# Kernel optimization log

Measured on AMD Instinct MI355X. Metric: run time of the kernel, lower is better.

The kernel has to match this reference:

```python
import jax, jax.numpy as jnp
import numpy as np

HIDDEN = 1024
HEADS = 16
HEAD_DIM = HIDDEN // HEADS
EPS = 1e-5


def setup_inputs() -> dict:
    key = jax.random.key(0)
    ks = jax.random.split(key, 9)
    B, S, H = 2, 2048, HIDDEN
    scale = 1.0 / np.sqrt(H)
    inp = {
        "hidden_states": jax.random.normal(ks[0], (B, S, H), dtype=jnp.float32),
        "Wq": jax.random.normal(ks[1], (H, H), dtype=jnp.float32) * scale,
        "bq": jnp.zeros((H,), jnp.float32),
        "Wk": jax.random.normal(ks[2], (H, H), dtype=jnp.float32) * scale,
        "bk": jnp.zeros((H,), jnp.float32),
        "Wv": jax.random.normal(ks[3], (H, H), dtype=jnp.float32) * scale,
        "bv": jnp.zeros((H,), jnp.float32),
        "Wo": jax.random.normal(ks[4], (H, H), dtype=jnp.float32) * scale,
        "bo": jnp.zeros((H,), jnp.float32),
        "gamma": jnp.ones((H,), jnp.float32),
        "beta": jnp.zeros((H,), jnp.float32),
    }
    return inp


def reference(hidden_states, Wq, bq, Wk, bk, Wv, bv, Wo, bo, gamma, beta):
    B, S, H = hidden_states.shape
    residual = hidden_states

    def shape(x):  # [B,S,H] -> [B,heads,S,head_dim]
        return x.reshape(B, S, HEADS, HEAD_DIM).transpose(0, 2, 1, 3)

    q = shape(hidden_states @ Wq + bq)
    k = shape(hidden_states @ Wk + bk)
    v = shape(hidden_states @ Wv + bv)

    scores = jnp.einsum("bhqd,bhkd->bhqk", q, k) / jnp.sqrt(
        jnp.asarray(HEAD_DIM, hidden_states.dtype))
    probs = jax.nn.softmax(scores, axis=-1)
    context = jnp.einsum("bhqk,bhkd->bhqd", probs, v)
    context = context.transpose(0, 2, 1, 3).reshape(B, S, H)

    output = context @ Wo + bo
    x = output + residual
    mu = jnp.mean(x, axis=-1, keepdims=True)
    var = jnp.mean(jnp.square(x - mu), axis=-1, keepdims=True)
    return (x - mu) * jax.lax.rsqrt(var + EPS) * gamma + beta
```

## Files before the change

kernel.cpp:

```cpp
#include <hip/hip_runtime.h>
#include <hip/hip_bf16.h>
#include <math.h>

#define HIDDEN 1024
#define HEADS 16
#define HEAD_DIM 64
#define EPS 1e-5f

typedef __attribute__((ext_vector_type(8))) short bf16x8;
typedef __attribute__((ext_vector_type(4))) float f32x4;

#if defined(__has_builtin)
#if __has_builtin(__builtin_amdgcn_exp2f)
#define EXP2(x) __builtin_amdgcn_exp2f(x)
#endif
#endif
#ifndef EXP2
#define EXP2(x) exp2f(x)
#endif

#define QSCALE 0.18033688011112042f

__device__ __forceinline__ short f2bf(float f) {
    union { float f; unsigned u; } v; v.f = f;
    unsigned r = v.u + 0x7fffu + ((v.u >> 16) & 1u);
    return (short)(r >> 16);
}

__device__ __forceinline__ void gl_lds16(const void* g, void* l) {
    __builtin_amdgcn_global_load_lds(
        (const __attribute__((address_space(1))) void*)g,
        (__attribute__((address_space(3))) void*)l, 16, 0, 0);
}

__global__ __launch_bounds__(256) void prep_kernel(
    const float* __restrict__ X,
    const float* __restrict__ Wq, const float* __restrict__ Wk,
    const float* __restrict__ Wv, const float* __restrict__ Wo,
    const float* __restrict__ bq, const float* __restrict__ bk,
    const float* __restrict__ bv,
    short* __restrict__ Xb, short* __restrict__ Wt3, short* __restrict__ Wot,
    float* __restrict__ b3)
{
    __shared__ short tile[32][33];
    const int id = blockIdx.x;
    if (id < 4096) {
        int i = id * 1024 + threadIdx.x * 4;
        float4 v = *(const float4*)(X + i);
        short o[4] = { f2bf(v.x), f2bf(v.y), f2bf(v.z), f2bf(v.w) };
        *(uint2*)(Xb + i) = *(uint2*)o;
    } else if (id < 8192) {
        int t = id - 4096;
        const int wsel = t >> 10; t &= 1023;
        const float* W = (wsel == 0) ? Wq : (wsel == 1) ? Wk : (wsel == 2) ? Wv : Wo;
        short* dst = (wsel < 3) ? (Wt3 + (size_t)wsel * 1024 * 1024) : Wot;
        const float scale = (wsel == 0) ? QSCALE : 1.0f;
        int n0 = (t & 31) * 32;
        int k0 = (t >> 5) * 32;
        int tx = threadIdx.x & 31;
        int ty = threadIdx.x >> 5;
        #pragma unroll
        for (int i = 0; i < 32; i += 8)
            tile[ty + i][tx] = f2bf(W[(size_t)(k0 + ty + i) * 1024 + n0 + tx] * scale);
        __syncthreads();
        #pragma unroll
        for (int i = 0; i < 32; i += 8)
            dst[(size_t)(n0 + ty + i) * 1024 + k0 + tx] = tile[tx][ty + i];
    } else {
        int i = (id - 8192) * 256 + threadIdx.x;
        if (i < 3072) {
            float v = (i < 1024) ? bq[i] * QSCALE
                    : (i < 2048) ? bk[i - 1024] : bv[i - 2048];
            b3[i] = v;
        }
    }
}

__global__ __launch_bounds__(256) void gemm_bt_mfma(
    const short* __restrict__ A, const short* __restrict__ Bt,
    const float* __restrict__ bias,
    void* __restrict__ C0, int ldc0,
    void* __restrict__ C1, int split_col, int ldc1, int v_transpose,
    const float* __restrict__ resid,
    int M, int N, int K, int out_bf16)
{
    __shared__ short As[128 * 32];
    __shared__ short Bs[128 * 32];
    const int tid = threadIdx.x;
    const int wave = tid >> 6, lane = tid & 63;
    const int ln16 = lane & 15, quad = lane >> 4;
    const int wm = (wave >> 1) * 64, wn = (wave & 1) * 64;
    const int brow = blockIdx.y * 128, bcol = blockIdx.x * 128;

    const int sr  = lane >> 2;
    const int scb = lane & 3;

    f32x4 acc[4][4];
    #pragma unroll
    for (int mt = 0; mt < 4; ++mt)
        #pragma unroll
        for (int nt = 0; nt < 4; ++nt) acc[mt][nt] = (f32x4){0.f, 0.f, 0.f, 0.f};

    for (int k0 = 0; k0 < K; k0 += 32) {
        __syncthreads();
        #pragma unroll
        for (int i = 0; i < 2; ++i) {
            int rb = i * 64 + wave * 16;
            int r  = rb + sr;
            int csrc = (scb ^ ((r >> 1) & 3)) * 8;
            gl_lds16(A  + (size_t)(brow + r) * K + k0 + csrc, &As[rb * 32]);
            gl_lds16(Bt + (size_t)(bcol + r) * K + k0 + csrc, &Bs[rb * 32]);
        }
        __syncthreads();

        bf16x8 af[4], bf[4];
        #pragma unroll
        for (int mt = 0; mt < 4; ++mt) {
            int r = wm + mt * 16 + ln16;
            af[mt] = *(const bf16x8*)&As[r * 32 + ((quad ^ ((r >> 1) & 3)) * 8)];
        }
        #pragma unroll
        for (int nt = 0; nt < 4; ++nt) {
            int r = wn + nt * 16 + ln16;
            bf[nt] = *(const bf16x8*)&Bs[r * 32 + ((quad ^ ((r >> 1) & 3)) * 8)];
        }
        #pragma unroll
        for (int mt = 0; mt < 4; ++mt)
            #pragma unroll
            for (int nt = 0; nt < 4; ++nt)
                acc[mt][nt] = __builtin_amdgcn_mfma_f32_16x16x32_bf16(
                    af[mt], bf[nt], acc[mt][nt], 0, 0, 0);
    }

    if (v_transpose && bcol >= split_col) {
        #pragma unroll
        for (int mt = 0; mt < 4; ++mt) {
            int row0 = brow + wm + mt * 16 + quad * 4;
            #pragma unroll
            for (int nt = 0; nt < 4; ++nt) {
                int col = bcol + wn + nt * 16 + ln16;
                int feat = col - split_col;
                float bz = bias[col];
                short pk[4];
                #pragma unroll
                for (int r = 0; r < 4; ++r) pk[r] = f2bf(acc[mt][nt][r] + bz);
                *(uint2*)((short*)C1 + (size_t)feat * ldc1 + row0) = *(uint2*)pk;
            }
        }
        return;
    }

    void* Cp = C0; int ld = ldc0; int coff = 0;
    if (bcol >= split_col) { Cp = C1; ld = ldc1; coff = split_col; }

    #pragma unroll
    for (int mt = 0; mt < 4; ++mt) {
        #pragma unroll
        for (int r = 0; r < 4; ++r) {
            int row = brow + wm + mt * 16 + quad * 4 + r;
            #pragma unroll
            for (int nt = 0; nt < 4; ++nt) {
                int col = bcol + wn + nt * 16 + ln16;
                float v = acc[mt][nt][r] + bias[col];
                if (resid) v += resid[(size_t)row * N + col];
                if (out_bf16) ((short*)Cp)[(size_t)row * ld + (col - coff)] = f2bf(v);
                else          ((float*)Cp)[(size_t)row * ld + (col - coff)] = v;
            }
        }
    }
}

__global__ __launch_bounds__(256) void attn_mfma_kernel(
    const short* __restrict__ QKb, const short* __restrict__ VT,
    short* __restrict__ Ctx)
{
    const int S = 2048;
    const int h = blockIdx.x, qt = blockIdx.y, b = blockIdx.z;
    const int tid = threadIdx.x;
    const int wave = tid >> 6, lane = tid & 63;
    const int ln16 = lane & 15, quad = lane >> 4;
    const int qh = wave >> 1, kh = wave & 1;

    __shared__ short Ks[2][64 * 64];
    __shared__ short Vs[2][64 * 64];
    __shared__ short Ps[256 * 72];
    __shared__ float Ls[128];

    const int qbase = b * S + qt * 128 + qh * 64;
    bf16x8 qfrag[4][2];
    #pragma unroll
    for (int qg = 0; qg < 4; ++qg)
        #pragma unroll
        for (int kb = 0; kb < 2; ++kb)
            qfrag[qg][kb] = *(const bf16x8*)(QKb +
                (size_t)(qbase + qg * 16 + ln16) * 2048 + h * 64 + kb * 32 + quad * 8);

    bf16x8 ones;
    #pragma unroll
    for (int j = 0; j < 8; ++j) ones[j] = (short)0x3F80;

    f32x4 of[4][4], lacc[4];
    #pragma unroll
    for (int qg = 0; qg < 4; ++qg) {
        lacc[qg] = (f32x4){0.f, 0.f, 0.f, 0.f};
        #pragma unroll
        for (int nt = 0; nt < 4; ++nt) of[qg][nt] = (f32x4){0.f, 0.f, 0.f, 0.f};
    }

    const int st  = wave >> 1;
    const int skv = wave & 1;
    const int sr  = lane >> 3;
    const int scb = lane & 7;

    for (int p = 0; p < 16; ++p) {
        __syncthreads();
        #pragma unroll
        for (int c = 0; c < 8; ++c) {
            int r = c * 8 + sr;
            int csrc = (scb ^ (r & 7)) * 8;
            int ktp = 2 * p + st;
            if (skv == 0) {
                gl_lds16(QKb + (size_t)(b * S + ktp * 64 + r) * 2048
                             + 1024 + h * 64 + csrc,
                         &Ks[st][c * 512]);
            } else {
                gl_lds16(VT + (size_t)(h * 64 + r) * 4096
                            + b * S + ktp * 64 + csrc,
                         &Vs[st][c * 512]);
            }
        }
        __syncthreads();

        #pragma unroll
        for (int nt = 0; nt < 4; ++nt) {
            bf16x8 kf[2];
            #pragma unroll
            for (int kb = 0; kb < 2; ++kb) {
                int r = nt * 16 + ln16;
                int cb = (kb * 4 + quad) ^ (r & 7);
                kf[kb] = *(const bf16x8*)&Ks[kh][r * 64 + cb * 8];
            }
            #pragma unroll
            for (int qg = 0; qg < 4; ++qg) {
                f32x4 a = (f32x4){0.f, 0.f, 0.f, 0.f};
                a = __builtin_amdgcn_mfma_f32_16x16x32_bf16(kf[0], qfrag[qg][0], a, 0, 0, 0);
                a = __builtin_amdgcn_mfma_f32_16x16x32_bf16(kf[1], qfrag[qg][1], a, 0, 0, 0);
                float p0 = EXP2(a[0]), p1 = EXP2(a[1]);
                float p2 = EXP2(a[2]), p3 = EXP2(a[3]);
                union { __hip_bfloat162 h2; unsigned u; } c01, c23;
                c01.h2 = __float22bfloat162_rn(make_float2(p0, p1));
                c23.h2 = __float22bfloat162_rn(make_float2(p2, p3));
                uint2 w; w.x = c01.u; w.y = c23.u;
                *(uint2*)&Ps[(wave * 64 + qg * 16 + ln16) * 72 + nt * 16 + quad * 4] = w;
            }
        }

        bf16x8 pf[4][2];
        #pragma unroll
        for (int qg = 0; qg < 4; ++qg)
            #pragma unroll
            for (int kb = 0; kb < 2; ++kb)
                pf[qg][kb] = *(const bf16x8*)
                    &Ps[(wave * 64 + qg * 16 + ln16) * 72 + kb * 32 + quad * 8];

        #pragma unroll
        for (int qg = 0; qg < 4; ++qg) {
            lacc[qg] = __builtin_amdgcn_mfma_f32_16x16x32_bf16(pf[qg][0], ones, lacc[qg], 0, 0, 0);
            lacc[qg] = __builtin_amdgcn_mfma_f32_16x16x32_bf16(pf[qg][1], ones, lacc[qg], 0, 0, 0);
        }
        #pragma unroll
        for (int nt = 0; nt < 4; ++nt) {
            bf16x8 vf[2];
            #pragma unroll
            for (int kb = 0; kb < 2; ++kb) {
                int r = nt * 16 + ln16;
                int cb = (kb * 4 + quad) ^ (r & 7);
                vf[kb] = *(const bf16x8*)&Vs[kh][r * 64 + cb * 8];
            }
            #pragma unroll
            for (int qg = 0; qg < 4; ++qg) {
                of[qg][nt] = __builtin_amdgcn_mfma_f32_16x16x32_bf16(pf[qg][0], vf[0], of[qg][nt], 0, 0, 0);
                of[qg][nt] = __builtin_amdgcn_mfma_f32_16x16x32_bf16(pf[qg][1], vf[1], of[qg][nt], 0, 0, 0);
            }
        }
    }

    float* Os = (float*)Ps;
    float* OsQ = Os + qh * (64 * 66);
    __syncthreads();
    if (kh == 1) {
        #pragma unroll
        for (int qg = 0; qg < 4; ++qg) {
            #pragma unroll
            for (int r = 0; r < 4; ++r) {
                int ql = qg * 16 + quad * 4 + r;
                #pragma unroll
                for (int nt = 0; nt < 4; ++nt)
                    OsQ[ql * 66 + nt * 16 + ln16] = of[qg][nt][r];
                if (ln16 == 0) Ls[qh * 64 + ql] = lacc[qg][r];
            }
        }
    }
    __syncthreads();
    if (kh == 0) {
        #pragma unroll
        for (int qg = 0; qg < 4; ++qg) {
            #pragma unroll
            for (int r = 0; r < 4; ++r) {
                int ql = qg * 16 + quad * 4 + r;
                float inv = 1.f / (lacc[qg][r] + Ls[qh * 64 + ql]);
                int row = qbase + ql;
                #pragma unroll
                for (int nt = 0; nt < 4; ++nt) {
                    float v = of[qg][nt][r] + OsQ[ql * 66 + nt * 16 + ln16];
                    Ctx[(size_t)row * 1024 + h * 64 + nt * 16 + ln16] = f2bf(v * inv);
                }
            }
        }
    }
}

__global__ __launch_bounds__(256) void resln_kernel(
    const float* __restrict__ xin, const float* __restrict__ gamma,
    const float* __restrict__ beta, float* __restrict__ out)
{
    const int row = blockIdx.x;
    const int tid = threadIdx.x;
    const int wid = tid >> 6, lane = tid & 63;
    __shared__ float red[8];

    float4 x = *(const float4*)(xin + (size_t)row * HIDDEN + tid * 4);
    float s = x.x + x.y + x.z + x.w;
    #pragma unroll
    for (int off = 32; off > 0; off >>= 1) s += __shfl_xor(s, off, 64);
    if (lane == 0) red[wid] = s;
    __syncthreads();
    float mu = (red[0] + red[1] + red[2] + red[3]) * (1.f / HIDDEN);

    float dx = x.x - mu, dy = x.y - mu, dz = x.z - mu, dw = x.w - mu;
    float v = dx * dx + dy * dy + dz * dz + dw * dw;
    #pragma unroll
    for (int off = 32; off > 0; off >>= 1) v += __shfl_xor(v, off, 64);
    if (lane == 0) red[4 + wid] = v;
    __syncthreads();
    float var = (red[4] + red[5] + red[6] + red[7]) * (1.f / HIDDEN);
    float rstd = rsqrtf(var + EPS);

    float4 g = *(const float4*)(gamma + tid * 4);
    float4 bt = *(const float4*)(beta + tid * 4);
    float4 o;
    o.x = dx * rstd * g.x + bt.x;
    o.y = dy * rstd * g.y + bt.y;
    o.z = dz * rstd * g.z + bt.z;
    o.w = dw * rstd * g.w + bt.w;
    *(float4*)(out + (size_t)row * HIDDEN + tid * 4) = o;
}

extern "C" void kernel_launch(void* const* d_in, const int* in_sizes, int n_in,
                              void* d_out, int out_size, void* d_ws, size_t ws_size,
                              hipStream_t stream)
{
    const float* X     = (const float*)d_in[0];
    const float* Wq    = (const float*)d_in[1];
    const float* bq    = (const float*)d_in[2];
    const float* Wk    = (const float*)d_in[3];
    const float* bk    = (const float*)d_in[4];
    const float* Wv    = (const float*)d_in[5];
    const float* bv    = (const float*)d_in[6];
    const float* Wo    = (const float*)d_in[7];
    const float* bo    = (const float*)d_in[8];
    const float* gamma = (const float*)d_in[9];
    const float* beta  = (const float*)d_in[10];
    float* out = (float*)d_out;

    const int B = 2, S = 2048;
    const int M = B * S;

    char* ws = (char*)d_ws;
    short* Xb  = (short*)(ws);
    short* Wot = (short*)(ws + (8ull << 20));
    short* Wt3 = (short*)(ws + (10ull << 20));
    float* b3  = (float*)(ws + (16ull << 20));
    short* QKb = (short*)(ws + (17ull << 20));
    float* Pj  = (float*)(ws + (17ull << 20));
    short* VT  = (short*)(ws + (33ull << 20));
    short* Ctx = (short*)(ws + (41ull << 20));

    dim3 blk(256);

    prep_kernel<<<dim3(8204), blk, 0, stream>>>(X, Wq, Wk, Wv, Wo, bq, bk, bv,
                                                Xb, Wt3, Wot, b3);

    dim3 qkvgrid(3072 / 128, M / 128);
    gemm_bt_mfma<<<qkvgrid, blk, 0, stream>>>(Xb, Wt3, b3,
                                              QKb, 2048, VT, 2048, 4096, 1,
                                              nullptr, M, 3072, HIDDEN, 1);

    dim3 agrid(HEADS, S / 128, B);
    attn_mfma_kernel<<<agrid, blk, 0, stream>>>(QKb, VT, Ctx);

    dim3 ogrid(HIDDEN / 128, M / 128);
    gemm_bt_mfma<<<ogrid, blk, 0, stream>>>(Ctx, Wot, bo,
                                            Pj, 1024, nullptr, 1 << 30, 0, 0,
                                            X, M, HIDDEN, HIDDEN, 0);

    resln_kernel<<<M, blk, 0, stream>>>(Pj, gamma, beta, out);
}
```

Measured before the change: 248.0 us.

## Deepen GEMM K-tile, remap blocks per XCD, split-K output projection, separate V transpose

The GEMM K tile grows from 32 to 64 with an 8-way XOR swizzle, which halves the barrier and loop iterations. Block ids are remapped so that each XCD handles a contiguous stripe of rows, to improve L2 locality. The output projection uses split-K across two slices, and the layernorm kernel sums the two partial results, raising block count for the 256-tile GEMM. The V transpose moves out of the GEMM epilogue into a separate LDS-tiled transpose kernel, so the GEMM writes coalesced rows, at the cost of an extra launch and an extra pass over V.

```diff
diff --git a/kernel.cpp b/kernel.cpp
--- a/kernel.cpp
+++ b/kernel.cpp
@@ -80,20 +80,32 @@
     const short* __restrict__ A, const short* __restrict__ Bt,
     const float* __restrict__ bias,
     void* __restrict__ C0, int ldc0,
-    void* __restrict__ C1, int split_col, int ldc1, int v_transpose,
+    void* __restrict__ C1, int split_col, int ldc1,
     const float* __restrict__ resid,
-    int M, int N, int K, int out_bf16)
-{
-    __shared__ short As[128 * 32];
-    __shared__ short Bs[128 * 32];
+    int M, int N, int K, int nbx, int klen, size_t slice_stride,
+    int out_bf16)
+{
+    __shared__ short As[128 * 64];
+    __shared__ short Bs[128 * 64];
     const int tid = threadIdx.x;
     const int wave = tid >> 6, lane = tid & 63;
     const int ln16 = lane & 15, quad = lane >> 4;
     const int wm = (wave >> 1) * 64, wn = (wave & 1) * 64;
-    const int brow = blockIdx.y * 128, bcol = blockIdx.x * 128;
-
-    const int sr  = lane >> 2;
-    const int scb = lane & 3;
+
+    const int id = blockIdx.x;
+    const int stripe = (M >> 7) >> 3;
+    const int xcd = id & 7;
+    const int s = id >> 3;
+    const int by = xcd * stripe + s / nbx;
+    const int bx = s % nbx;
+    const int brow = by * 128, bcol = bx * 128;
+
+    const int kbase = blockIdx.y * klen;
+    const float* bias_s  = (blockIdx.y == 0) ? bias  : nullptr;
+    const float* resid_s = (blockIdx.y == 0) ? resid : nullptr;
+
+    const int sr8  = lane >> 3;
+    const int scb8 = lane & 7;
 
     f32x4 acc[4][4];
     #pragma unroll
@@ -101,72 +113,85 @@
         #pragma unroll
         for (int nt = 0; nt < 4; ++nt) acc[mt][nt] = (f32x4){0.f, 0.f, 0.f, 0.f};
 
-    for (int k0 = 0; k0 < K; k0 += 32) {
+    for (int k0 = 0; k0 < klen; k0 += 64) {
         __syncthreads();
         #pragma unroll
-        for (int i = 0; i < 2; ++i) {
-            int rb = i * 64 + wave * 16;
-            int r  = rb + sr;
-            int csrc = (scb ^ ((r >> 1) & 3)) * 8;
-            gl_lds16(A  + (size_t)(brow + r) * K + k0 + csrc, &As[rb * 32]);
-            gl_lds16(Bt + (size_t)(bcol + r) * K + k0 + csrc, &Bs[rb * 32]);
+        for (int i = 0; i < 4; ++i) {
+            int c = wave * 4 + i;
+            int r = c * 8 + sr8;
+            int csrc = (scb8 ^ (r & 7)) * 8;
+            gl_lds16(A  + (size_t)(brow + r) * K + kbase + k0 + csrc, &As[c * 512]);
+            gl_lds16(Bt + (size_t)(bcol + r) * K + kbase + k0 + csrc, &Bs[c * 512]);
         }
         __syncthreads();
 
-        bf16x8 af[4], bf[4];
-        #pragma unroll
-        for (int mt = 0; mt < 4; ++mt) {
-            int r = wm + mt * 16 + ln16;
-            af[mt] = *(const bf16x8*)&As[r * 32 + ((quad ^ ((r >> 1) & 3)) * 8)];
-        }
-        #pragma unroll
-        for (int nt = 0; nt < 4; ++nt) {
-            int r = wn + nt * 16 + ln16;
-            bf[nt] = *(const bf16x8*)&Bs[r * 32 + ((quad ^ ((r >> 1) & 3)) * 8)];
-        }
-        #pragma unroll
-        for (int mt = 0; mt < 4; ++mt)
-            #pragma unroll
-            for (int nt = 0; nt < 4; ++nt)
-                acc[mt][nt] = __builtin_amdgcn_mfma_f32_16x16x32_bf16(
-                    af[mt], bf[nt], acc[mt][nt], 0, 0, 0);
-    }
-
-    if (v_transpose && bcol >= split_col) {
-        #pragma unroll
-        for (int mt = 0; mt < 4; ++mt) {
-            int row0 = brow + wm + mt * 16 + quad * 4;
+        #pragma unroll
+        for (int kb = 0; kb < 2; ++kb) {
+            bf16x8 af[4], bf[4];
+            #pragma unroll
+            for (int mt = 0; mt < 4; ++mt) {
+                int r = wm + mt * 16 + ln16;
+                af[mt] = *(const bf16x8*)&As[r * 64 + (((kb * 4 + quad) ^ (r & 7)) * 8)];
+            }
+            #pragma unroll
+            for (int nt = 0; nt < 4; ++nt) {
+                int r = wn + nt * 16 + ln16;
+                bf[nt] = *(const bf16x8*)&Bs[r * 64 + (((kb * 4 + quad) ^ (r & 7)) * 8)];
+            }
+            #pragma unroll
+            for (int mt = 0; mt < 4; ++mt)
+                #pragma unroll
+                for (int nt = 0; nt < 4; ++nt)
+                    acc[mt][nt] = __builtin_amdgcn_mfma_f32_16x16x32_bf16(
+                        af[mt], bf[nt], acc[mt][nt], 0, 0, 0);
+        }
+    }
+
+    void* Cp = C0; int ld = ldc0; int coff = 0;
+    if (bcol >= split_col) { Cp = C1; ld = ldc1; coff = split_col; }
+    if (!out_bf16) Cp = (float*)Cp + (size_t)blockIdx.y * slice_stride;
+    else           Cp = (short*)Cp + (size_t)blockIdx.y * slice_stride;
+
+    #pragma unroll
+    for (int mt = 0; mt < 4; ++mt) {
+        #pragma unroll
+        for (int r = 0; r < 4; ++r) {
+            int row = brow + wm + mt * 16 + quad * 4 + r;
             #pragma unroll
             for (int nt = 0; nt < 4; ++nt) {
                 int col = bcol + wn + nt * 16 + ln16;
-                int feat = col - split_col;
-                float bz = bias[col];
-                short pk[4];
-                #pragma unroll
-                for (int r = 0; r < 4; ++r) pk[r] = f2bf(acc[mt][nt][r] + bz);
-                *(uint2*)((short*)C1 + (size_t)feat * ldc1 + row0) = *(uint2*)pk;
-            }
-        }
-        return;
-    }
-
-    void* Cp = C0; int ld = ldc0; int coff = 0;
-    if (bcol >= split_col) { Cp = C1; ld = ldc1; coff = split_col; }
-
-    #pragma unroll
-    for (int mt = 0; mt < 4; ++mt) {
-        #pragma unroll
-        for (int r = 0; r < 4; ++r) {
-            int row = brow + wm + mt * 16 + quad * 4 + r;
-            #pragma unroll
-            for (int nt = 0; nt < 4; ++nt) {
-                int col = bcol + wn + nt * 16 + ln16;
-                float v = acc[mt][nt][r] + bias[col];
-                if (resid) v += resid[(size_t)row * N + col];
+                float v = acc[mt][nt][r];
+                if (bias_s)  v += bias_s[col];
+                if (resid_s) v += resid_s[(size_t)row * N + col];
                 if (out_bf16) ((short*)Cp)[(size_t)row * ld + (col - coff)] = f2bf(v);
                 else          ((float*)Cp)[(size_t)row * ld + (col - coff)] = v;
             }
         }
+    }
+}
+
+__global__ __launch_bounds__(256) void vtranspose_kernel(
+    const short* __restrict__ Vb, short* __restrict__ VT)
+{
+    __shared__ short t[64][72];
+    const int c0 = blockIdx.x * 64;
+    const int r0 = blockIdx.y * 64;
+    const int tid = threadIdx.x;
+    #pragma unroll
+    for (int i = 0; i < 2; ++i) {
+        int idx = tid + i * 256;
+        int r = idx >> 3, cc = (idx & 7) * 8;
+        *(uint4*)&t[r][cc] = *(const uint4*)(Vb + (size_t)(r0 + r) * 1024 + c0 + cc);
+    }
+    __syncthreads();
+    #pragma unroll
+    for (int i = 0; i < 2; ++i) {
+        int idx = tid + i * 256;
+        int c = idx >> 3, rr = (idx & 7) * 8;
+        short tmp[8];
+        #pragma unroll
+        for (int j = 0; j < 8; ++j) tmp[j] = t[rr + j][c];
+        *(uint4*)(VT + (size_t)(c0 + c) * 4096 + r0 + rr) = *(uint4*)tmp;
     }
 }
 
@@ -321,15 +346,20 @@
 }
 
 __global__ __launch_bounds__(256) void resln_kernel(
-    const float* __restrict__ xin, const float* __restrict__ gamma,
-    const float* __restrict__ beta, float* __restrict__ out)
+    const float* __restrict__ p0, const float* __restrict__ p1,
+    const float* __restrict__ gamma, const float* __restrict__ beta,
+    float* __restrict__ out)
 {
     const int row = blockIdx.x;
     const int tid = threadIdx.x;
     const int wid = tid >> 6, lane = tid & 63;
     __shared__ float red[8];
 
-    float4 x = *(const float4*)(xin + (size_t)row * HIDDEN + tid * 4);
+    float4 a = *(const float4*)(p0 + (size_t)row * HIDDEN + tid * 4);
+    float4 c = *(const float4*)(p1 + (size_t)row * HIDDEN + tid * 4);
+    float4 x;
+    x.x = a.x + c.x; x.y = a.y + c.y; x.z = a.z + c.z; x.w = a.w + c.w;
+
     float s = x.x + x.y + x.z + x.w;
     #pragma unroll
     for (int off = 32; off > 0; off >>= 1) s += __shfl_xor(s, off, 64);
@@ -378,31 +408,34 @@
 
     char* ws = (char*)d_ws;
     short* Xb  = (short*)(ws);
+    short* Ctx = (short*)(ws);
     short* Wot = (short*)(ws + (8ull << 20));
     short* Wt3 = (short*)(ws + (10ull << 20));
     float* b3  = (float*)(ws + (16ull << 20));
     short* QKb = (short*)(ws + (17ull << 20));
-    float* Pj  = (float*)(ws + (17ull << 20));
-    short* VT  = (short*)(ws + (33ull << 20));
-    short* Ctx = (short*)(ws + (41ull << 20));
+    float* Pj0 = (float*)(ws + (17ull << 20));
+    short* Vb  = (short*)(ws + (33ull << 20));
+    float* Pj1 = (float*)(ws + (33ull << 20));
+    short* VT  = (short*)(ws + (41ull << 20));
 
     dim3 blk(256);
 
     prep_kernel<<<dim3(8204), blk, 0, stream>>>(X, Wq, Wk, Wv, Wo, bq, bk, bv,
                                                 Xb, Wt3, Wot, b3);
 
-    dim3 qkvgrid(3072 / 128, M / 128);
-    gemm_bt_mfma<<<qkvgrid, blk, 0, stream>>>(Xb, Wt3, b3,
-                                              QKb, 2048, VT, 2048, 4096, 1,
-                                              nullptr, M, 3072, HIDDEN, 1);
+    gemm_bt_mfma<<<dim3(768, 1), blk, 0, stream>>>(
+        Xb, Wt3, b3, QKb, 2048, Vb, 2048, 1024, nullptr,
+        M, 3072, 1024, 24, 1024, 0, 1);
+
+    vtranspose_kernel<<<dim3(16, 64), blk, 0, stream>>>(Vb, VT);
 
     dim3 agrid(HEADS, S / 128, B);
     attn_mfma_kernel<<<agrid, blk, 0, stream>>>(QKb, VT, Ctx);
 
-    dim3 ogrid(HIDDEN / 128, M / 128);
-    gemm_bt_mfma<<<ogrid, blk, 0, stream>>>(Ctx, Wot, bo,
-                                            Pj, 1024, nullptr, 1 << 30, 0, 0,
-                                            X, M, HIDDEN, HIDDEN, 0);
-
-    resln_kernel<<<M, blk, 0, stream>>>(Pj, gamma, beta, out);
-}
+    gemm_bt_mfma<<<dim3(256, 2), blk, 0, stream>>>(
+        Ctx, Wot, bo, Pj0, 1024, nullptr, 1 << 30, 0, X,
+        M, 1024, 1024, 8, 512,
+        (size_t)M * HIDDEN, 0);
+
+    resln_kernel<<<M, blk, 0, stream>>>(Pj0, Pj1, gamma, beta, out);
+}
```

Measured after the change: 264.5 us. 1.07x slower.
